# Kernel optimization log

Measured on AMD Instinct MI355X. Metric: run time of the kernel, lower is better.

## Reference

```python
import jax, jax.numpy as jnp
import numpy as np
import math

EPS = 1e-5

def _ln(x, g, b):
    m = jnp.mean(x, axis=-1, keepdims=True)
    v = jnp.mean((x - m) ** 2, axis=-1, keepdims=True)
    return (x - m) * jax.lax.rsqrt(v + EPS) * g + b

def _heads(t, H):
    B, T, C = t.shape
    return t.reshape(B, T, H, C // H).transpose(0, 2, 1, 3)  # [B,H,T,D]

def _merge(t):
    B, H, T, D = t.shape
    return t.transpose(0, 2, 1, 3).reshape(B, T, H * D)

def _self_attn(x, w, b, pw, pb, H):
    B, T, C = x.shape
    q, k, v = jnp.split(x @ w + b, 3, axis=-1)
    q, k, v = _heads(q, H), _heads(k, H), _heads(v, H)
    D = C // H
    att = jnp.einsum('bhqd,bhkd->bhqk', q, k) * (1.0 / math.sqrt(D))
    causal = jnp.tril(jnp.ones((T, T), bool))
    att = jnp.where(causal[None, None], att, jnp.float32(-jnp.inf))
    att = jax.nn.softmax(att, axis=-1)
    out = _merge(jnp.einsum('bhqk,bhkd->bhqd', att, v))
    return out @ pw + pb

def _cross_attn(enc, dec, w, b, pw, pb, H):
    B, Td, C = dec.shape
    q_dec = jnp.split(dec @ w + b, 3, axis=-1)[0]
    _, k_enc, v_enc = jnp.split(enc @ w + b, 3, axis=-1)
    q = _heads(q_dec, H); k = _heads(k_enc, H); v = _heads(v_enc, H)
    D = C // H
    att = jnp.einsum('bhqd,bhkd->bhqk', q, k) * (1.0 / math.sqrt(D))
    att = jax.nn.softmax(att, axis=-1)
    out = _merge(jnp.einsum('bhqk,bhkd->bhqd', att, v))
    return out @ pw + pb

def _block(x, encoder_embd,
           ln1_g, ln1_b, ln2_g, ln2_b, ln3_g, ln3_b,
           attn_w, attn_b, aproj_w, aproj_b,
           ca_w, ca_b, caproj_w, caproj_b,
           fc_w, fc_b, mproj_w, mproj_b,
           down_w, down_b, up_w, up_b, H=16):
    x = x + _self_attn(_ln(x, ln1_g, ln1_b), attn_w, attn_b, aproj_w, aproj_b, H)
    x = x + _cross_attn(encoder_embd, _ln(x, ln2_g, ln2_b), ca_w, ca_b, caproj_w, caproj_b, H)
    h = jax.nn.gelu(_ln(x, ln3_g, ln3_b) @ fc_w + fc_b, approximate=True) @ mproj_w + mproj_b
    adapt = jax.nn.gelu(h @ down_w + down_b, approximate=True) @ up_w + up_b + h  # Adapter residual
    return x + adapt


def setup_inputs() -> dict:
    key = jax.random.key(0)
    ks = jax.random.split(key, 12)
    B, T, Te, C, H = 4, 1024, 257, 1024, 16
    s = 0.02
    f32 = jnp.float32
    return {
        'x': jax.random.normal(ks[0], (B, T, C), f32),
        'encoder_embd': jax.random.normal(ks[1], (B, Te, C), f32),
        'prefix_embd': jnp.zeros((B, 1, C), f32),
        'ln1_g': jnp.ones((C,), f32), 'ln1_b': jnp.zeros((C,), f32),
        'ln2_g': jnp.ones((C,), f32), 'ln2_b': jnp.zeros((C,), f32),
        'ln3_g': jnp.ones((C,), f32), 'ln3_b': jnp.zeros((C,), f32),
        'attn_w': jax.random.normal(ks[2], (C, 3 * C), f32) * s,
        'attn_b': jnp.zeros((3 * C,), f32),
        'aproj_w': jax.random.normal(ks[3], (C, C), f32) * s,
        'aproj_b': jnp.zeros((C,), f32),
        'ca_w': jax.random.normal(ks[4], (C, 3 * C), f32) * s,
        'ca_b': jnp.zeros((3 * C,), f32),
        'caproj_w': jax.random.normal(ks[5], (C, C), f32) * s,
        'caproj_b': jnp.zeros((C,), f32),
        'fc_w': jax.random.normal(ks[6], (C, 4 * C), f32) * s,
        'fc_b': jnp.zeros((4 * C,), f32),
        'mproj_w': jax.random.normal(ks[7], (4 * C, C), f32) * s,
        'mproj_b': jnp.zeros((C,), f32),
        'down_w': jax.random.normal(ks[8], (C, C // 4), f32) * s,
        'down_b': jnp.zeros((C // 4,), f32),
        'up_w': jax.random.normal(ks[9], (C // 4, C), f32) * s,
        'up_b': jnp.zeros((C,), f32),
    }


def reference(x, encoder_embd, prefix_embd,
              ln1_g, ln1_b, ln2_g, ln2_b, ln3_g, ln3_b,
              attn_w, attn_b, aproj_w, aproj_b,
              ca_w, ca_b, caproj_w, caproj_b,
              fc_w, fc_b, mproj_w, mproj_b,
              down_w, down_b, up_w, up_b):
    # prefix_embd unused (peft='adapter')
    return _block(x, encoder_embd,
                  ln1_g, ln1_b, ln2_g, ln2_b, ln3_g, ln3_b,
                  attn_w, attn_b, aproj_w, aproj_b,
                  ca_w, ca_b, caproj_w, caproj_b,
                  fc_w, fc_b, mproj_w, mproj_b,
                  down_w, down_b, up_w, up_b)
```

## Files before the change

kernel.cpp:

```cpp
#include <hip/hip_runtime.h>

typedef __attribute__((ext_vector_type(8))) short short8v;
typedef __attribute__((ext_vector_type(8))) unsigned short ushort8v;
typedef __attribute__((ext_vector_type(4))) float f32x4;

__device__ __forceinline__ unsigned short f2b(float f) {
  unsigned int u = __float_as_uint(f);
  unsigned int r = (u + 0x7FFFu + ((u >> 16) & 1u)) >> 16;
  return (unsigned short)r;
}
__device__ __forceinline__ float b2f(unsigned short h) {
  return __uint_as_float(((unsigned int)h) << 16);
}
__device__ __forceinline__ float gelu_f(float x) {
  float z = 0.7978845608028654f * (x + 0.044715f * x * x * x);
  float e = __expf(2.0f * z);
  float t = 1.0f - 2.0f / (e + 1.0f);
  return 0.5f * x * (1.0f + t);
}
__device__ __forceinline__ void gload16(const void* g, void* l) {
  __builtin_amdgcn_global_load_lds((const __attribute__((address_space(1))) unsigned int*)g,
                                   (__attribute__((address_space(3))) unsigned int*)l,
                                   16, 0, 0);
}

__global__ __launch_bounds__(256) void k_transpose_cvt(const float* __restrict__ w,
                                                       unsigned short* __restrict__ wt,
                                                       int K, int N) {
  __shared__ float tile[64][65];
  int tn = blockIdx.x * 64, tk = blockIdx.y * 64;
  int c = threadIdx.x & 63, r0 = threadIdx.x >> 6;
#pragma unroll
  for (int p = 0; p < 16; ++p) {
    int r = r0 + p * 4;
    tile[r][c] = w[(size_t)(tk + r) * N + tn + c];
  }
  __syncthreads();
#pragma unroll
  for (int p = 0; p < 16; ++p) {
    int r = r0 + p * 4;
    wt[(size_t)(tn + r) * K + tk + c] = f2b(tile[c][r]);
  }
}

__global__ void k_cvt_bf16(const float* __restrict__ in, unsigned short* __restrict__ out, int n) {
  int i = blockIdx.x * 256 + threadIdx.x;
  if (i < n) out[i] = f2b(in[i]);
}

__global__ __launch_bounds__(256) void k_ln(const float* __restrict__ in,
                                            const float* __restrict__ g,
                                            const float* __restrict__ b,
                                            unsigned short* __restrict__ out) {
  int row = blockIdx.x;
  const float* x = in + (size_t)row * 1024;
  int t = threadIdx.x;
  float v0 = x[t], v1 = x[t + 256], v2 = x[t + 512], v3 = x[t + 768];
  float s = v0 + v1 + v2 + v3;
  float s2 = v0 * v0 + v1 * v1 + v2 * v2 + v3 * v3;
#pragma unroll
  for (int m = 1; m < 64; m <<= 1) { s += __shfl_xor(s, m); s2 += __shfl_xor(s2, m); }
  __shared__ float rs[4], rs2[4];
  int w = t >> 6;
  if ((t & 63) == 0) { rs[w] = s; rs2[w] = s2; }
  __syncthreads();
  s = rs[0] + rs[1] + rs[2] + rs[3];
  s2 = rs2[0] + rs2[1] + rs2[2] + rs2[3];
  float mean = s * (1.0f / 1024.0f);
  float var = s2 * (1.0f / 1024.0f) - mean * mean;
  float rinv = rsqrtf(var + 1e-5f);
  unsigned short* o = out + (size_t)row * 1024;
  o[t]       = f2b((v0 - mean) * rinv * g[t]       + b[t]);
  o[t + 256] = f2b((v1 - mean) * rinv * g[t + 256] + b[t + 256]);
  o[t + 512] = f2b((v2 - mean) * rinv * g[t + 512] + b[t + 512]);
  o[t + 768] = f2b((v3 - mean) * rinv * g[t + 768] + b[t + 768]);
}

template <bool GELU>
__global__ __launch_bounds__(512, 2) void k_g256p(
    const unsigned short* __restrict__ A, int lda,
    const unsigned short* __restrict__ W, int ldw,
    const float* __restrict__ bias,
    unsigned short* __restrict__ outB, int ldo, int K) {
  __shared__ unsigned short lds[65536];
  const int t = threadIdx.x;
  const int tileM = blockIdx.y * 256, tileN = blockIdx.x * 256;
  const int lane = t & 63, w = t >> 6;
  const int wm = w >> 2, wn = w & 3;
  const int lr16 = lane & 15, kc4 = lane >> 4;

  const int row1 = t >> 2, row2 = row1 + 128, cs = t & 3;
  const int c1 = (cs ^ ((row1 >> 1) & 3)) * 8;
  const int c2 = (cs ^ ((row2 >> 1) & 3)) * 8;
  const unsigned short* a1 = A + (size_t)(tileM + row1) * lda + c1;
  const unsigned short* a2 = A + (size_t)(tileM + row2) * lda + c2;
  const unsigned short* w1 = W + (size_t)(tileN + row1) * ldw + c1;
  const unsigned short* w2 = W + (size_t)(tileN + row2) * ldw + c2;

  f32x4 acc[8][4];
#pragma unroll
  for (int i = 0; i < 8; ++i)
#pragma unroll
    for (int j = 0; j < 4; ++j) acc[i][j] = f32x4{0.f, 0.f, 0.f, 0.f};

  const int nt = K >> 6;
  const int H = nt * 4;

#define STAGE_HALF(h)                                                        \
  do {                                                                       \
    int tile_s = (h) >> 2, id = (h) & 3, slot = (h) & 7;                     \
    int koff = tile_s * 64 + (id >> 1) * 32;                                 \
    unsigned short* dst = &lds[slot * 8192 + t * 8];                         \
    if (id & 1) { gload16(w1 + koff, dst); gload16(w2 + koff, dst + 4096); } \
    else        { gload16(a1 + koff, dst); gload16(a2 + koff, dst + 4096); } \
  } while (0)

#pragma unroll
  for (int h = 0; h < 6; ++h) { if (h < H) STAGE_HALF(h); }
  asm volatile("s_waitcnt vmcnt(8)" ::: "memory");
  __builtin_amdgcn_s_barrier();

  for (int T = 0; T < nt; ++T) {
    short8v bfr[4];
#pragma unroll
    for (int q = 0; q < 4; ++q) {
      const int ks = q >> 1, mh = q & 1;
      const int aslot = (((T & 1) * 4 + 2 * ks)) * 8192;
      const int bslot = (((T & 1) * 4 + 2 * ks + 1)) * 8192;
      if (mh == 0) {
#pragma unroll
        for (int n = 0; n < 4; ++n) {
          int r = wn * 64 + n * 16 + lr16;
          bfr[n] = *(const short8v*)&lds[bslot + r * 32 + (kc4 ^ ((r >> 1) & 3)) * 8];
        }
      }
      short8v aF[4];
#pragma unroll
      for (int m4 = 0; m4 < 4; ++m4) {
        int r = wm * 128 + mh * 64 + m4 * 16 + lr16;
        aF[m4] = *(const short8v*)&lds[aslot + r * 32 + (kc4 ^ ((r >> 1) & 3)) * 8];
      }
      int h = 4 * T + q + 6;
      if (h < H) STAGE_HALF(h);
      if (q & 1) {
        if (T < nt - 2)       asm volatile("s_waitcnt vmcnt(8)" ::: "memory");
        else if (T == nt - 2) {
          if (q == 1)         asm volatile("s_waitcnt vmcnt(4)" ::: "memory");
          else                asm volatile("s_waitcnt vmcnt(0)" ::: "memory");
        }
      }
      __builtin_amdgcn_s_barrier();
      asm volatile("s_waitcnt lgkmcnt(0)" ::: "memory");
      __builtin_amdgcn_sched_barrier(0);
      __builtin_amdgcn_s_setprio(1);
#pragma unroll
      for (int m4 = 0; m4 < 4; ++m4)
#pragma unroll
        for (int n = 0; n < 4; ++n)
          acc[mh * 4 + m4][n] =
              __builtin_amdgcn_mfma_f32_16x16x32_bf16(aF[m4], bfr[n], acc[mh * 4 + m4][n], 0, 0, 0);
      __builtin_amdgcn_s_setprio(0);
      __builtin_amdgcn_sched_barrier(0);
      __builtin_amdgcn_s_barrier();
    }
  }
#undef STAGE_HALF

#pragma unroll
  for (int mi = 0; mi < 8; ++mi) {
#pragma unroll
    for (int n = 0; n < 4; ++n) {
      int col = tileN + wn * 64 + n * 16 + lr16;
      float bv = bias[col];
#pragma unroll
      for (int qi = 0; qi < 4; ++qi) {
        int row = tileM + wm * 128 + mi * 16 + kc4 * 4 + qi;
        float v = acc[mi][n][qi] + bv;
        if (GELU) v = gelu_f(v);
        outB[(size_t)row * ldo + col] = f2b(v);
      }
    }
  }
}

template <bool GELU, bool WF32, bool WBF16, int NRES, bool RES1B>
__global__ __launch_bounds__(256) void k_g128(
    const unsigned short* __restrict__ A, int lda,
    const unsigned short* __restrict__ W, int ldw,
    const float* __restrict__ bias,
    const float* __restrict__ res1, const unsigned short* __restrict__ res1b,
    const float* __restrict__ res2,
    float* __restrict__ outF, unsigned short* __restrict__ outB,
    int M, int N, int K) {
  __shared__ unsigned short lds[32768];
  const int t = threadIdx.x;
  const int tileM = blockIdx.y * 128, tileN = blockIdx.x * 128;
  const int lane = t & 63, w = t >> 6;
  const int wm = (w >> 1) * 64, wn = (w & 1) * 64;
  const int lr16 = lane & 15, kc4 = lane >> 4;

  const int row1 = t >> 2, row2 = row1 + 64, cs = t & 3;
  const int c1 = (cs ^ ((row1 >> 1) & 3)) * 8;
  const int c2 = (cs ^ ((row2 >> 1) & 3)) * 8;
  int gr1 = tileM + row1; if (gr1 >= M) gr1 = M - 1;
  int gr2 = tileM + row2; if (gr2 >= M) gr2 = M - 1;
  const unsigned short* a1 = A + (size_t)gr1 * lda + c1;
  const unsigned short* a2 = A + (size_t)gr2 * lda + c2;
  const unsigned short* w1 = W + (size_t)(tileN + row1) * ldw + c1;
  const unsigned short* w2 = W + (size_t)(tileN + row2) * ldw + c2;

  f32x4 acc[4][4];
#pragma unroll
  for (int i = 0; i < 4; ++i)
#pragma unroll
    for (int j = 0; j < 4; ++j) acc[i][j] = f32x4{0.f, 0.f, 0.f, 0.f};

  const int nt = K >> 6;

#define STAGE128(b, koff)                                  \
  do {                                                     \
    unsigned short* dst = &lds[(b) * 16384 + t * 8];       \
    gload16(a1 + (koff), dst);                             \
    gload16(a2 + (koff), dst + 2048);                      \
    gload16(a1 + (koff) + 32, dst + 4096);                 \
    gload16(a2 + (koff) + 32, dst + 6144);                 \
    gload16(w1 + (koff), dst + 8192);                      \
    gload16(w2 + (koff), dst + 10240);                     \
    gload16(w1 + (koff) + 32, dst + 12288);                \
    gload16(w2 + (koff) + 32, dst + 14336);                \
  } while (0)

  STAGE128(0, 0);
  asm volatile("s_waitcnt vmcnt(0)" ::: "memory");
  __builtin_amdgcn_s_barrier();

  for (int T = 0; T < nt; ++T) {
    if (T + 1 < nt) STAGE128((T + 1) & 1, (T + 1) * 64);
    const unsigned short* buf = &lds[(T & 1) * 16384];
#pragma unroll
    for (int s = 0; s < 2; ++s) {
      const unsigned short* ab = buf + s * 4096;
      const unsigned short* bb = buf + 8192 + s * 4096;
      short8v bfr[4];
#pragma unroll
      for (int n = 0; n < 4; ++n) {
        int r = wn + n * 16 + lr16;
        bfr[n] = *(const short8v*)&bb[r * 32 + (kc4 ^ ((r >> 1) & 3)) * 8];
      }
#pragma unroll
      for (int mi = 0; mi < 4; ++mi) {
        int r = wm + mi * 16 + lr16;
        short8v af = *(const short8v*)&ab[r * 32 + (kc4 ^ ((r >> 1) & 3)) * 8];
#pragma unroll
        for (int n = 0; n < 4; ++n)
          acc[mi][n] = __builtin_amdgcn_mfma_f32_16x16x32_bf16(af, bfr[n], acc[mi][n], 0, 0, 0);
      }
    }
    if (T + 1 < nt) {
      asm volatile("s_waitcnt vmcnt(0)" ::: "memory");
      __builtin_amdgcn_s_barrier();
    }
  }
#undef STAGE128

#pragma unroll
  for (int mi = 0; mi < 4; ++mi) {
#pragma unroll
    for (int n = 0; n < 4; ++n) {
      int col = tileN + wn + n * 16 + lr16;
      float bv = bias[col];
#pragma unroll
      for (int qi = 0; qi < 4; ++qi) {
        int row = tileM + wm + mi * 16 + kc4 * 4 + qi;
        if (row < M) {
          float v = acc[mi][n][qi] + bv;
          if (GELU) v = gelu_f(v);
          size_t o = (size_t)row * N + col;
          if (NRES >= 1) v += RES1B ? b2f(res1b[o]) : res1[o];
          if (NRES >= 2) v += res2[o];
          if (WF32) outF[o] = v;
          if (WBF16) outB[o] = f2b(v);
        }
      }
    }
  }
}

__global__ __launch_bounds__(256) void k_vtrans(const unsigned short* __restrict__ src,
                                                int src_stride, int src_off, int TB,
                                                unsigned short* __restrict__ dst, int dst_tstride) {
  __shared__ unsigned short tile[64][72];
  int tb = blockIdx.x, bh = blockIdx.y;
  int b = bh >> 4, h = bh & 15;
  int t = threadIdx.x;
  int r = t >> 2, c0 = (t & 3) * 16;
  int tok = tb * 64 + r; if (tok >= TB) tok = TB - 1;
  const unsigned short* s = src + (size_t)(b * TB + tok) * src_stride + src_off + h * 64 + c0;
  *(ushort8v*)&tile[r][c0] = *(const ushort8v*)s;
  *(ushort8v*)&tile[r][c0 + 8] = *(const ushort8v*)(s + 8);
  __syncthreads();
  unsigned short tmp[16];
#pragma unroll
  for (int j = 0; j < 16; ++j) tmp[j] = tile[c0 + j][r];
  unsigned short* dp = dst + ((size_t)bh * 64 + r) * dst_tstride + tb * 64 + c0;
  *(ushort8v*)dp = *(const ushort8v*)&tmp[0];
  *(ushort8v*)(dp + 8) = *(const ushort8v*)&tmp[8];
}

template <bool CAUSAL>
__global__ __launch_bounds__(256) void k_attn(
    const unsigned short* __restrict__ Qb, int q_stride,
    const unsigned short* __restrict__ Kb, int k_stride, int k_off, int TKR,
    const unsigned short* __restrict__ Vt, int vt_tstride,
    unsigned short* __restrict__ out, int Tk) {
  __shared__ unsigned short Kl[64 * 72];
  __shared__ unsigned short Vl[64 * 72];
  __shared__ unsigned short Pl[4][16 * 72];
  int qb = blockIdx.x, bh = blockIdx.y;
  int b = bh >> 4, h = bh & 15;
  int t = threadIdx.x, lane = t & 63, w = t >> 6;
  int g = lane >> 4, lc = lane & 15;

  int qrow_g = qb * 64 + w * 16 + lc;
  const unsigned short* qp = Qb + (size_t)(b * 1024 + qrow_g) * q_stride + h * 64 + g * 8;
  short8v aq0 = *(const short8v*)qp;
  short8v aq1 = *(const short8v*)(qp + 32);

  f32x4 o[4];
  float m_[4], l_[4];
#pragma unroll
  for (int dt = 0; dt < 4; ++dt) o[dt] = f32x4{0.f, 0.f, 0.f, 0.f};
#pragma unroll
  for (int r = 0; r < 4; ++r) { m_[r] = -3.0e38f; l_[r] = 0.0f; }

  int srow = t >> 2;
  int sc = (t & 3) * 16;
  int ntiles = CAUSAL ? (qb + 1) : ((Tk + 63) >> 6);

  for (int kt = 0; kt < ntiles; ++kt) {
    __syncthreads();
    {
      int kg = kt * 64 + srow;
      if (!CAUSAL && kg >= Tk) kg = Tk - 1;
      const unsigned short* ks = Kb + (size_t)(b * TKR + kg) * k_stride + k_off + h * 64 + sc;
      *(ushort8v*)&Kl[srow * 72 + sc]     = *(const ushort8v*)ks;
      *(ushort8v*)&Kl[srow * 72 + sc + 8] = *(const ushort8v*)(ks + 8);
      const unsigned short* vs = Vt + ((size_t)bh * 64 + srow) * vt_tstride + kt * 64 + sc;
      *(ushort8v*)&Vl[srow * 72 + sc]     = *(const ushort8v*)vs;
      *(ushort8v*)&Vl[srow * 72 + sc + 8] = *(const ushort8v*)(vs + 8);
    }
    __syncthreads();

    f32x4 s[4];
#pragma unroll
    for (int jt = 0; jt < 4; ++jt) {
      short8v bk0 = *(const short8v*)&Kl[(jt * 16 + lc) * 72 + g * 8];
      short8v bk1 = *(const short8v*)&Kl[(jt * 16 + lc) * 72 + g * 8 + 32];
      f32x4 acc = f32x4{0.f, 0.f, 0.f, 0.f};
      acc = __builtin_amdgcn_mfma_f32_16x16x32_bf16(aq0, bk0, acc, 0, 0, 0);
      acc = __builtin_amdgcn_mfma_f32_16x16x32_bf16(aq1, bk1, acc, 0, 0, 0);
      s[jt] = acc;
    }
#pragma unroll
    for (int jt = 0; jt < 4; ++jt)
#pragma unroll
      for (int r = 0; r < 4; ++r) {
        float sv = s[jt][r] * 0.125f;
        bool masked = CAUSAL ? (kt == qb && (jt * 16 + lc) > (w * 16 + g * 4 + r))
                             : (kt * 64 + jt * 16 + lc >= Tk);
        s[jt][r] = masked ? -3.0e38f : sv;
      }
    float f[4];
#pragma unroll
    for (int r = 0; r < 4; ++r) {
      float mx = fmaxf(fmaxf(s[0][r], s[1][r]), fmaxf(s[2][r], s[3][r]));
      mx = fmaxf(mx, __shfl_xor(mx, 1));
      mx = fmaxf(mx, __shfl_xor(mx, 2));
      mx = fmaxf(mx, __shfl_xor(mx, 4));
      mx = fmaxf(mx, __shfl_xor(mx, 8));
      float mnew = fmaxf(m_[r], mx);
      f[r] = __expf(m_[r] - mnew);
      m_[r] = mnew;
      float rsum = 0.0f;
#pragma unroll
      for (int jt = 0; jt < 4; ++jt) {
        float p = __expf(s[jt][r] - mnew);
        s[jt][r] = p;
        rsum += p;
      }
      rsum += __shfl_xor(rsum, 1);
      rsum += __shfl_xor(rsum, 2);
      rsum += __shfl_xor(rsum, 4);
      rsum += __shfl_xor(rsum, 8);
      l_[r] = l_[r] * f[r] + rsum;
    }
#pragma unroll
    for (int dt = 0; dt < 4; ++dt)
#pragma unroll
      for (int r = 0; r < 4; ++r) o[dt][r] *= f[r];
#pragma unroll
    for (int jt = 0; jt < 4; ++jt)
#pragma unroll
      for (int r = 0; r < 4; ++r)
        Pl[w][(g * 4 + r) * 72 + jt * 16 + lc] = f2b(s[jt][r]);
    short8v ap0 = *(const short8v*)&Pl[w][lc * 72 + g * 8];
    short8v ap1 = *(const short8v*)&Pl[w][lc * 72 + g * 8 + 32];
#pragma unroll
    for (int dt = 0; dt < 4; ++dt) {
      short8v bv0 = *(const short8v*)&Vl[(dt * 16 + lc) * 72 + g * 8];
      short8v bv1 = *(const short8v*)&Vl[(dt * 16 + lc) * 72 + g * 8 + 32];
      o[dt] = __builtin_amdgcn_mfma_f32_16x16x32_bf16(ap0, bv0, o[dt], 0, 0, 0);
      o[dt] = __builtin_amdgcn_mfma_f32_16x16x32_bf16(ap1, bv1, o[dt], 0, 0, 0);
    }
  }
  size_t orow = (size_t)(b * 1024 + qb * 64 + w * 16) * 1024 + h * 64;
#pragma unroll
  for (int r = 0; r < 4; ++r) {
    float inv = 1.0f / l_[r];
#pragma unroll
    for (int dt = 0; dt < 4; ++dt)
      out[orow + (size_t)(g * 4 + r) * 1024 + dt * 16 + lc] = f2b(o[dt][r] * inv);
  }
}

extern "C" void kernel_launch(void* const* d_in, const int* in_sizes, int n_in,
                              void* d_out, int out_size, void* d_ws, size_t ws_size,
                              hipStream_t stream) {
  (void)in_sizes; (void)n_in; (void)out_size; (void)ws_size;
  const float* x       = (const float*)d_in[0];
  const float* enc     = (const float*)d_in[1];
  const float* ln1_g   = (const float*)d_in[3];
  const float* ln1_b   = (const float*)d_in[4];
  const float* ln2_g   = (const float*)d_in[5];
  const float* ln2_b   = (const float*)d_in[6];
  const float* ln3_g   = (const float*)d_in[7];
  const float* ln3_b   = (const float*)d_in[8];
  const float* attn_w  = (const float*)d_in[9];
  const float* attn_b  = (const float*)d_in[10];
  const float* aproj_w = (const float*)d_in[11];
  const float* aproj_b = (const float*)d_in[12];
  const float* ca_w    = (const float*)d_in[13];
  const float* ca_b    = (const float*)d_in[14];
  const float* caproj_w= (const float*)d_in[15];
  const float* caproj_b= (const float*)d_in[16];
  const float* fc_w    = (const float*)d_in[17];
  const float* fc_b    = (const float*)d_in[18];
  const float* mproj_w = (const float*)d_in[19];
  const float* mproj_b = (const float*)d_in[20];
  const float* down_w  = (const float*)d_in[21];
  const float* down_b  = (const float*)d_in[22];
  const float* up_w    = (const float*)d_in[23];
  const float* up_b    = (const float*)d_in[24];
  float* out = (float*)d_out;
  char* ws = (char*)d_ws;

  const size_t O_WATTN = 0, O_WAPROJ = 6291456, O_WCA = 8388608, O_WCAPROJ = 14680064,
               O_WFC = 16777216, O_WMPROJ = 25165824, O_WDOWN = 33554432, O_WUP = 34078720,
               O_ENC = 34603008, O_LN = 36708352, O_BIG = 45096960,
               O_XRES = 78651392, O_ATTN = 112205824;

  unsigned short* wt_attn   = (unsigned short*)(ws + O_WATTN);
  unsigned short* wt_aproj  = (unsigned short*)(ws + O_WAPROJ);
  unsigned short* wt_ca     = (unsigned short*)(ws + O_WCA);
  unsigned short* wt_caproj = (unsigned short*)(ws + O_WCAPROJ);
  unsigned short* wt_fc     = (unsigned short*)(ws + O_WFC);
  unsigned short* wt_mproj  = (unsigned short*)(ws + O_WMPROJ);
  unsigned short* wt_down   = (unsigned short*)(ws + O_WDOWN);
  unsigned short* wt_up     = (unsigned short*)(ws + O_WUP);
  unsigned short* encbf     = (unsigned short*)(ws + O_ENC);
  unsigned short* lnout     = (unsigned short*)(ws + O_LN);
  unsigned short* hbf       = (unsigned short*)(ws + O_LN);
  unsigned short* qkvb      = (unsigned short*)(ws + O_BIG);
  unsigned short* vt_self   = (unsigned short*)(ws + O_BIG + 25165824);
  unsigned short* q2b       = (unsigned short*)(ws + O_BIG);
  unsigned short* kvb       = (unsigned short*)(ws + O_BIG + 8388608);
  unsigned short* vt_cross  = (unsigned short*)(ws + O_BIG + 12599296);
  unsigned short* caout     = (unsigned short*)(ws + O_BIG + 15220736);
  unsigned short* fcout     = (unsigned short*)(ws + O_BIG);
  float*          xres      = (float*)(ws + O_XRES);
  unsigned short* attnout   = (unsigned short*)(ws + O_ATTN);
  unsigned short* dmid      = (unsigned short*)(ws + O_ATTN);

  dim3 blk(256);
  dim3 blk5(512);

  k_transpose_cvt<<<dim3(48, 16), blk, 0, stream>>>(attn_w,  wt_attn,   1024, 3072);
  k_transpose_cvt<<<dim3(16, 16), blk, 0, stream>>>(aproj_w, wt_aproj,  1024, 1024);
  k_transpose_cvt<<<dim3(48, 16), blk, 0, stream>>>(ca_w,    wt_ca,     1024, 3072);
  k_transpose_cvt<<<dim3(16, 16), blk, 0, stream>>>(caproj_w,wt_caproj, 1024, 1024);
  k_transpose_cvt<<<dim3(64, 16), blk, 0, stream>>>(fc_w,    wt_fc,     1024, 4096);
  k_transpose_cvt<<<dim3(16, 64), blk, 0, stream>>>(mproj_w, wt_mproj,  4096, 1024);
  k_transpose_cvt<<<dim3(4, 16),  blk, 0, stream>>>(down_w,  wt_down,   1024, 256);
  k_transpose_cvt<<<dim3(16, 4),  blk, 0, stream>>>(up_w,    wt_up,     256,  1024);
  k_cvt_bf16<<<dim3(4112), blk, 0, stream>>>(enc, encbf, 1028 * 1024);

  k_ln<<<dim3(4096), blk, 0, stream>>>(x, ln1_g, ln1_b, lnout);
  k_g256p<false><<<dim3(12, 16), blk5, 0, stream>>>(
      lnout, 1024, wt_attn, 1024, attn_b, qkvb, 3072, 1024);
  k_vtrans<<<dim3(16, 64), blk, 0, stream>>>(qkvb, 3072, 2048, 1024, vt_self, 1024);
  k_attn<true><<<dim3(16, 64), blk, 0, stream>>>(
      qkvb, 3072, qkvb, 3072, 1024, 1024, vt_self, 1024, attnout, 1024);
  k_g128<false, true, false, 1, false><<<dim3(8, 32), blk, 0, stream>>>(
      attnout, 1024, wt_aproj, 1024, aproj_b, x, nullptr, nullptr, xres, nullptr,
      4096, 1024, 1024);

  k_ln<<<dim3(4096), blk, 0, stream>>>(xres, ln2_g, ln2_b, lnout);
  k_g128<false, false, true, 0, false><<<dim3(8, 32), blk, 0, stream>>>(
      lnout, 1024, wt_ca, 1024, ca_b, nullptr, nullptr, nullptr, nullptr, q2b,
      4096, 1024, 1024);
  k_g128<false, false, true, 0, false><<<dim3(16, 9), blk, 0, stream>>>(
      encbf, 1024, wt_ca + (size_t)1024 * 1024, 1024, ca_b + 1024, nullptr, nullptr,
      nullptr, nullptr, kvb, 1028, 2048, 1024);
  k_vtrans<<<dim3(5, 64), blk, 0, stream>>>(kvb, 2048, 1024, 257, vt_cross, 320);
  k_attn<false><<<dim3(16, 64), blk, 0, stream>>>(
      q2b, 1024, kvb, 2048, 0, 257, vt_cross, 320, caout, 257);
  k_g128<false, true, false, 1, false><<<dim3(8, 32), blk, 0, stream>>>(
      caout, 1024, wt_caproj, 1024, caproj_b, xres, nullptr, nullptr, xres, nullptr,
      4096, 1024, 1024);

  k_ln<<<dim3(4096), blk, 0, stream>>>(xres, ln3_g, ln3_b, lnout);
  k_g256p<true><<<dim3(16, 16), blk5, 0, stream>>>(
      lnout, 1024, wt_fc, 1024, fc_b, fcout, 4096, 1024);
  k_g128<false, false, true, 0, false><<<dim3(8, 32), blk, 0, stream>>>(
      fcout, 4096, wt_mproj, 4096, mproj_b, nullptr, nullptr, nullptr, nullptr, hbf,
      4096, 1024, 4096);

  k_g128<true, false, true, 0, false><<<dim3(2, 32), blk, 0, stream>>>(
      hbf, 1024, wt_down, 1024, down_b, nullptr, nullptr, nullptr, nullptr, dmid,
      4096, 256, 1024);
  k_g128<false, true, false, 2, true><<<dim3(8, 32), blk, 0, stream>>>(
      dmid, 256, wt_up, 256, up_b, nullptr, hbf, xres, out, nullptr,
      4096, 1024, 256);
}
```

Baseline: 498.9 us.

## Fuse weight prep into one launch, add XCD block swizzle and nontemporal stores

Merges the eight weight transpose-convert launches and the encoder bf16 conversion into one kernel that dispatches on block index, and vectorises the encoder conversion. GEMM and attention grids become 1D and are remapped with an XCD-aware swizzle, so blocks sharing tiles land on the same chiplet's L2. Most output stores become nontemporal. The nontemporal hint may hurt when a later kernel immediately rereads those outputs, such as the LN outputs feeding the GEMMs.

```diff
diff --git a/kernel.cpp b/kernel.cpp
--- a/kernel.cpp
+++ b/kernel.cpp
@@ -2,6 +2,7 @@
 
 typedef __attribute__((ext_vector_type(8))) short short8v;
 typedef __attribute__((ext_vector_type(8))) unsigned short ushort8v;
+typedef __attribute__((ext_vector_type(4))) unsigned short ushort4v;
 typedef __attribute__((ext_vector_type(4))) float f32x4;
 
 __device__ __forceinline__ unsigned short f2b(float f) {
@@ -23,13 +24,54 @@
                                    (__attribute__((address_space(3))) unsigned int*)l,
                                    16, 0, 0);
 }
-
-__global__ __launch_bounds__(256) void k_transpose_cvt(const float* __restrict__ w,
-                                                       unsigned short* __restrict__ wt,
-                                                       int K, int N) {
+__device__ __forceinline__ void nts_u16(unsigned short* p, unsigned short v) {
+  __builtin_nontemporal_store(v, p);
+}
+__device__ __forceinline__ void nts_f32(float* p, float v) {
+  __builtin_nontemporal_store(v, p);
+}
+__device__ __forceinline__ void nts_u16x8(unsigned short* p, ushort8v v) {
+  __builtin_nontemporal_store(v, (ushort8v*)p);
+}
+__device__ __forceinline__ int xcd_swz(int wgid, int nwg) {
+  int q = nwg >> 3, r = nwg & 7;
+  int xcd = wgid & 7, idx = wgid >> 3;
+  return (xcd < r ? xcd * (q + 1) : r * (q + 1) + (xcd - r) * q) + idx;
+}
+
+__global__ __launch_bounds__(256) void k_wprep(
+    const float* aw, unsigned short* awt,
+    const float* apw, unsigned short* apwt,
+    const float* cw, unsigned short* cwt,
+    const float* cpw, unsigned short* cpwt,
+    const float* fw, unsigned short* fwt,
+    const float* mw, unsigned short* mwt,
+    const float* dw, unsigned short* dwt,
+    const float* uw, unsigned short* uwt,
+    const float* enc, unsigned short* encb) {
   __shared__ float tile[64][65];
-  int tn = blockIdx.x * 64, tk = blockIdx.y * 64;
-  int c = threadIdx.x & 63, r0 = threadIdx.x >> 6;
+  int bid = blockIdx.x, t = threadIdx.x;
+  const float* w; unsigned short* wt; int K, N, gx, l;
+  if      (bid < 768)  { w = aw;  wt = awt;  K = 1024; N = 3072; gx = 48; l = bid; }
+  else if (bid < 1024) { w = apw; wt = apwt; K = 1024; N = 1024; gx = 16; l = bid - 768; }
+  else if (bid < 1792) { w = cw;  wt = cwt;  K = 1024; N = 3072; gx = 48; l = bid - 1024; }
+  else if (bid < 2048) { w = cpw; wt = cpwt; K = 1024; N = 1024; gx = 16; l = bid - 1792; }
+  else if (bid < 3072) { w = fw;  wt = fwt;  K = 1024; N = 4096; gx = 64; l = bid - 2048; }
+  else if (bid < 4096) { w = mw;  wt = mwt;  K = 4096; N = 1024; gx = 16; l = bid - 3072; }
+  else if (bid < 4160) { w = dw;  wt = dwt;  K = 1024; N = 256;  gx = 4;  l = bid - 4096; }
+  else if (bid < 4224) { w = uw;  wt = uwt;  K = 256;  N = 1024; gx = 16; l = bid - 4160; }
+  else {
+    size_t i = ((size_t)(bid - 4224) * 256 + t) * 4;
+    f32x4 v = *(const f32x4*)&enc[i];
+    ushort4v o;
+#pragma unroll
+    for (int j = 0; j < 4; ++j) o[j] = f2b(v[j]);
+    __builtin_nontemporal_store(o, (ushort4v*)&encb[i]);
+    return;
+  }
+  int bx = l % gx, by = l / gx;
+  int tn = bx * 64, tk = by * 64;
+  int c = t & 63, r0 = t >> 6;
 #pragma unroll
   for (int p = 0; p < 16; ++p) {
     int r = r0 + p * 4;
@@ -39,13 +81,8 @@
 #pragma unroll
   for (int p = 0; p < 16; ++p) {
     int r = r0 + p * 4;
-    wt[(size_t)(tn + r) * K + tk + c] = f2b(tile[c][r]);
-  }
-}
-
-__global__ void k_cvt_bf16(const float* __restrict__ in, unsigned short* __restrict__ out, int n) {
-  int i = blockIdx.x * 256 + threadIdx.x;
-  if (i < n) out[i] = f2b(in[i]);
+    nts_u16(&wt[(size_t)(tn + r) * K + tk + c], f2b(tile[c][r]));
+  }
 }
 
 __global__ __launch_bounds__(256) void k_ln(const float* __restrict__ in,
@@ -70,10 +107,10 @@
   float var = s2 * (1.0f / 1024.0f) - mean * mean;
   float rinv = rsqrtf(var + 1e-5f);
   unsigned short* o = out + (size_t)row * 1024;
-  o[t]       = f2b((v0 - mean) * rinv * g[t]       + b[t]);
-  o[t + 256] = f2b((v1 - mean) * rinv * g[t + 256] + b[t + 256]);
-  o[t + 512] = f2b((v2 - mean) * rinv * g[t + 512] + b[t + 512]);
-  o[t + 768] = f2b((v3 - mean) * rinv * g[t + 768] + b[t + 768]);
+  nts_u16(&o[t],       f2b((v0 - mean) * rinv * g[t]       + b[t]));
+  nts_u16(&o[t + 256], f2b((v1 - mean) * rinv * g[t + 256] + b[t + 256]));
+  nts_u16(&o[t + 512], f2b((v2 - mean) * rinv * g[t + 512] + b[t + 512]));
+  nts_u16(&o[t + 768], f2b((v3 - mean) * rinv * g[t + 768] + b[t + 768]));
 }
 
 template <bool GELU>
@@ -81,10 +118,11 @@
     const unsigned short* __restrict__ A, int lda,
     const unsigned short* __restrict__ W, int ldw,
     const float* __restrict__ bias,
-    unsigned short* __restrict__ outB, int ldo, int K) {
+    unsigned short* __restrict__ outB, int ldo, int K, int nbx) {
   __shared__ unsigned short lds[65536];
   const int t = threadIdx.x;
-  const int tileM = blockIdx.y * 256, tileN = blockIdx.x * 256;
+  const int swz = xcd_swz(blockIdx.x, gridDim.x);
+  const int tileM = (swz / nbx) * 256, tileN = (swz % nbx) * 256;
   const int lane = t & 63, w = t >> 6;
   const int wm = w >> 2, wn = w & 3;
   const int lr16 = lane & 15, kc4 = lane >> 4;
@@ -177,7 +215,7 @@
         int row = tileM + wm * 128 + mi * 16 + kc4 * 4 + qi;
         float v = acc[mi][n][qi] + bv;
         if (GELU) v = gelu_f(v);
-        outB[(size_t)row * ldo + col] = f2b(v);
+        nts_u16(&outB[(size_t)row * ldo + col], f2b(v));
       }
     }
   }
@@ -191,10 +229,11 @@
     const float* __restrict__ res1, const unsigned short* __restrict__ res1b,
     const float* __restrict__ res2,
     float* __restrict__ outF, unsigned short* __restrict__ outB,
-    int M, int N, int K) {
+    int M, int N, int K, int nbx) {
   __shared__ unsigned short lds[32768];
   const int t = threadIdx.x;
-  const int tileM = blockIdx.y * 128, tileN = blockIdx.x * 128;
+  const int swz = xcd_swz(blockIdx.x, gridDim.x);
+  const int tileM = (swz / nbx) * 128, tileN = (swz % nbx) * 128;
   const int lane = t & 63, w = t >> 6;
   const int wm = (w >> 1) * 64, wn = (w & 1) * 64;
   const int lr16 = lane & 15, kc4 = lane >> 4;
@@ -278,8 +317,8 @@
           size_t o = (size_t)row * N + col;
           if (NRES >= 1) v += RES1B ? b2f(res1b[o]) : res1[o];
           if (NRES >= 2) v += res2[o];
-          if (WF32) outF[o] = v;
-          if (WBF16) outB[o] = f2b(v);
+          if (WF32) nts_f32(&outF[o], v);
+          if (WBF16) nts_u16(&outB[o], f2b(v));
         }
       }
     }
@@ -303,8 +342,8 @@
 #pragma unroll
   for (int j = 0; j < 16; ++j) tmp[j] = tile[c0 + j][r];
   unsigned short* dp = dst + ((size_t)bh * 64 + r) * dst_tstride + tb * 64 + c0;
-  *(ushort8v*)dp = *(const ushort8v*)&tmp[0];
-  *(ushort8v*)(dp + 8) = *(const ushort8v*)&tmp[8];
+  nts_u16x8(dp, *(const ushort8v*)&tmp[0]);
+  nts_u16x8(dp + 8, *(const ushort8v*)&tmp[8]);
 }
 
 template <bool CAUSAL>
@@ -316,7 +355,8 @@
   __shared__ unsigned short Kl[64 * 72];
   __shared__ unsigned short Vl[64 * 72];
   __shared__ unsigned short Pl[4][16 * 72];
-  int qb = blockIdx.x, bh = blockIdx.y;
+  const int swz = xcd_swz(blockIdx.x, gridDim.x);
+  int qb = swz & 15, bh = swz >> 4;
   int b = bh >> 4, h = bh & 15;
   int t = threadIdx.x, lane = t & 63, w = t >> 6;
   int g = lane >> 4, lc = lane & 15;
@@ -419,7 +459,7 @@
     float inv = 1.0f / l_[r];
 #pragma unroll
     for (int dt = 0; dt < 4; ++dt)
-      out[orow + (size_t)(g * 4 + r) * 1024 + dt * 16 + lc] = f2b(o[dt][r] * inv);
+      nts_u16(&out[orow + (size_t)(g * 4 + r) * 1024 + dt * 16 + lc], f2b(o[dt][r] * inv));
   }
 }
 
@@ -484,51 +524,45 @@
   dim3 blk(256);
   dim3 blk5(512);
 
-  k_transpose_cvt<<<dim3(48, 16), blk, 0, stream>>>(attn_w,  wt_attn,   1024, 3072);
-  k_transpose_cvt<<<dim3(16, 16), blk, 0, stream>>>(aproj_w, wt_aproj,  1024, 1024);
-  k_transpose_cvt<<<dim3(48, 16), blk, 0, stream>>>(ca_w,    wt_ca,     1024, 3072);
-  k_transpose_cvt<<<dim3(16, 16), blk, 0, stream>>>(caproj_w,wt_caproj, 1024, 1024);
-  k_transpose_cvt<<<dim3(64, 16), blk, 0, stream>>>(fc_w,    wt_fc,     1024, 4096);
-  k_transpose_cvt<<<dim3(16, 64), blk, 0, stream>>>(mproj_w, wt_mproj,  4096, 1024);
-  k_transpose_cvt<<<dim3(4, 16),  blk, 0, stream>>>(down_w,  wt_down,   1024, 256);
-  k_transpose_cvt<<<dim3(16, 4),  blk, 0, stream>>>(up_w,    wt_up,     256,  1024);
-  k_cvt_bf16<<<dim3(4112), blk, 0, stream>>>(enc, encbf, 1028 * 1024);
+  k_wprep<<<dim3(5252), blk, 0, stream>>>(
+      attn_w, wt_attn, aproj_w, wt_aproj, ca_w, wt_ca, caproj_w, wt_caproj,
+      fc_w, wt_fc, mproj_w, wt_mproj, down_w, wt_down, up_w, wt_up, enc, encbf);
 
   k_ln<<<dim3(4096), blk, 0, stream>>>(x, ln1_g, ln1_b, lnout);
-  k_g256p<false><<<dim3(12, 16), blk5, 0, stream>>>(
-      lnout, 1024, wt_attn, 1024, attn_b, qkvb, 3072, 1024);
+  k_g256p<false><<<dim3(192), blk5, 0, stream>>>(
+      lnout, 1024, wt_attn, 1024, attn_b, qkvb, 3072, 1024, 12);
   k_vtrans<<<dim3(16, 64), blk, 0, stream>>>(qkvb, 3072, 2048, 1024, vt_self, 1024);
-  k_attn<true><<<dim3(16, 64), blk, 0, stream>>>(
+  k_attn<true><<<dim3(1024), blk, 0, stream>>>(
       qkvb, 3072, qkvb, 3072, 1024, 1024, vt_self, 1024, attnout, 1024);
-  k_g128<false, true, false, 1, false><<<dim3(8, 32), blk, 0, stream>>>(
+  k_g128<false, true, false, 1, false><<<dim3(256), blk, 0, stream>>>(
       attnout, 1024, wt_aproj, 1024, aproj_b, x, nullptr, nullptr, xres, nullptr,
-      4096, 1024, 1024);
+      4096, 1024, 1024, 8);
 
   k_ln<<<dim3(4096), blk, 0, stream>>>(xres, ln2_g, ln2_b, lnout);
-  k_g128<false, false, true, 0, false><<<dim3(8, 32), blk, 0, stream>>>(
+  k_g128<false, false, true, 0, false><<<dim3(256), blk, 0, stream>>>(
       lnout, 1024, wt_ca, 1024, ca_b, nullptr, nullptr, nullptr, nullptr, q2b,
-      4096, 1024, 1024);
-  k_g128<false, false, true, 0, false><<<dim3(16, 9), blk, 0, stream>>>(
+      4096, 1024, 1024, 8);
+  k_g128<false, false, true, 0, false><<<dim3(144), blk, 0, stream>>>(
       encbf, 1024, wt_ca + (size_t)1024 * 1024, 1024, ca_b + 1024, nullptr, nullptr,
-      nullptr, nullptr, kvb, 1028, 2048, 1024);
+      nullptr, nullptr, kvb, 1028, 2048, 1024, 16);
   k_vtrans<<<dim3(5, 64), blk, 0, stream>>>(kvb, 2048, 1024, 257, vt_cross, 320);
-  k_attn<false><<<dim3(16, 64), blk, 0, stream>>>(
+  k_attn<false><<<dim3(1024), blk, 0, stream>>>(
       q2b, 1024, kvb, 2048, 0, 257, vt_cross, 320, caout, 257);
-  k_g128<false, true, false, 1, false><<<dim3(8, 32), blk, 0, stream>>>(
+  k_g128<false, true, false, 1, false><<<dim3(256), blk, 0, stream>>>(
       caout, 1024, wt_caproj, 1024, caproj_b, xres, nullptr, nullptr, xres, nullptr,
-      4096, 1024, 1024);
+      4096, 1024, 1024, 8);
 
   k_ln<<<dim3(4096), blk, 0, stream>>>(xres, ln3_g, ln3_b, lnout);
-  k_g256p<true><<<dim3(16, 16), blk5, 0, stream>>>(
-      lnout, 1024, wt_fc, 1024, fc_b, fcout, 4096, 1024);
-  k_g128<false, false, true, 0, false><<<dim3(8, 32), blk, 0, stream>>>(
+  k_g256p<true><<<dim3(256), blk5, 0, stream>>>(
+      lnout, 1024, wt_fc, 1024, fc_b, fcout, 4096, 1024, 16);
+  k_g128<false, false, true, 0, false><<<dim3(256), blk, 0, stream>>>(
       fcout, 4096, wt_mproj, 4096, mproj_b, nullptr, nullptr, nullptr, nullptr, hbf,
-      4096, 1024, 4096);
-
-  k_g128<true, false, true, 0, false><<<dim3(2, 32), blk, 0, stream>>>(
+      4096, 1024, 4096, 8);
+
+  k_g128<true, false, true, 0, false><<<dim3(64), blk, 0, stream>>>(
       hbf, 1024, wt_down, 1024, down_b, nullptr, nullptr, nullptr, nullptr, dmid,
-      4096, 256, 1024);
-  k_g128<false, true, false, 2, true><<<dim3(8, 32), blk, 0, stream>>>(
+      4096, 256, 1024, 2);
+  k_g128<false, true, false, 2, true><<<dim3(256), blk, 0, stream>>>(
       dmid, 256, wt_up, 256, up_b, nullptr, hbf, xres, out, nullptr,
-      4096, 1024, 256);
-}
+      4096, 1024, 256, 8);
+}
```

New measurement: 499.5 us. No clear change (+0.1%).
